# Kernel optimization log

Measured on AMD Instinct MI355X. Metric: run time of the kernel, lower is better.

The kernel has to match this reference:

```python
import jax, jax.numpy as jnp
import numpy as np

FAR = 10.0
RAST = 256          # rast_size default
ORIG_W, ORIG_H = 256.0, 256.0  # orig_size default
CHUNK = 32          # faces processed per scan step
EPS = 1e-9


def _project(vertices, K, R, t, dist):
    # persp projection with lens distortion; vertices [B,V,3] -> [B,V,3] (u,v in [-1,1], z depth)
    v = jnp.einsum('bvj,bij->bvi', vertices, R) + t
    x, y, z = v[..., 0], v[..., 1], v[..., 2]
    x_ = x / (z + EPS)
    y_ = y / (z + EPS)
    k1, k2, p1, p2, k3 = (dist[:, None, i] for i in range(5))
    r2 = x_ * x_ + y_ * y_  # == r**2 in original (r = sqrt(x_^2+y_^2))
    radial = 1.0 + k1 * r2 + k2 * r2 ** 2 + k3 * r2 ** 3
    x__ = x_ * radial + 2.0 * p1 * x_ * y_ + p2 * (r2 + 2.0 * x_ ** 2)
    y__ = y_ * radial + p1 * (r2 + 2.0 * y_ ** 2) + 2.0 * p2 * x_ * y_
    pts = jnp.stack([x__, y__, jnp.ones_like(z)], axis=-1)
    pts = jnp.einsum('bvj,bij->bvi', pts, K)
    u, vv = pts[..., 0], pts[..., 1]
    vv = ORIG_H - vv
    u = 2.0 * (u - ORIG_W / 2.0) / ORIG_W
    vv = 2.0 * (vv - ORIG_H / 2.0) / ORIG_H
    return jnp.stack([u, vv, z], axis=-1)


def _rasterize(fverts):
    # fverts: [B,F,3,3] per-face screen-space vertices (u,v,z). Z-buffer depth raster + coverage mask.
    B, F = fverts.shape[0], fverts.shape[1]
    pad = (-F) % CHUNK
    fv = jnp.pad(fverts, ((0, 0), (0, pad), (0, 0), (0, 0)))  # padded faces are degenerate (den==0)
    nc = (F + pad) // CHUNK
    fv = fv.reshape(B, nc, CHUNK, 3, 3).transpose(1, 0, 2, 3, 4)  # [nc,B,CHUNK,3,3]
    # pixel centers in [-1,1]; row i top-to-bottom maps to y = -1..1 (consistent with flipped v)
    g = 2.0 * (jnp.arange(RAST, dtype=jnp.float32) + 0.5) / RAST - 1.0
    X = g[None, None, None, :]   # cols
    Y = g[None, None, :, None]   # rows

    def body(carry, ch):
        zbuf, cover = carry
        e = lambda i, j: ch[:, :, i, j][:, :, None, None]
        ax, ay, az = e(0, 0), e(0, 1), e(0, 2)
        bx, by, bz = e(1, 0), e(1, 1), e(1, 2)
        cx, cy, cz = e(2, 0), e(2, 1), e(2, 2)
        den = (bx - ax) * (cy - ay) - (by - ay) * (cx - ax)
        ok = jnp.abs(den) > 1e-8
        den_s = jnp.where(ok, den, 1.0)
        # barycentric coords of each pixel wrt this face (signed; fill_back provides both windings)
        w0 = ((by - cy) * (X - cx) + (cx - bx) * (Y - cy)) / den_s
        w1 = ((cy - ay) * (X - cx) + (ax - cx) * (Y - cy)) / den_s
        w2 = 1.0 - w0 - w1
        zs = lambda zz: jnp.where(zz > 1e-8, zz, 1.0)
        inv = w0 / zs(az) + w1 / zs(bz) + w2 / zs(cz)  # perspective-correct 1/z interp
        valid = ok & (w0 >= 0) & (w1 >= 0) & (w2 >= 0)
        valid = valid & (az > 1e-8) & (bz > 1e-8) & (cz > 1e-8) & (inv > 1e-8)
        zp = 1.0 / jnp.where(valid, inv, 1.0)
        zc = jnp.min(jnp.where(valid, zp, FAR), axis=1)  # nearest face in this chunk [B,S,S]
        return (jnp.minimum(zbuf, zc), cover | jnp.any(valid, axis=1)), None

    zbuf0 = jnp.full((B, RAST, RAST), FAR, dtype=jnp.float32)
    cov0 = jnp.zeros((B, RAST, RAST), dtype=bool)
    (zbuf, cover), _ = jax.lax.scan(body, (zbuf0, cov0), fv)
    return zbuf, cover


def _normalize_depth(img, far):
    img_inf = (img == far).astype(jnp.float32)
    img_no_back = (1.0 - img_inf) * img
    img_max = img_no_back.max(axis=1, keepdims=True).max(axis=2, keepdims=True)
    img_min = img.min(axis=1, keepdims=True).min(axis=2, keepdims=True)
    nd = (img_max - img) / (img_max - img_min + 1e-4)
    return jnp.clip(nd, 0.0, 1.0)


def _forward(vertices, faces, intr, R, t, dist_coeffs):
    # fill_back=True: append faces with reversed vertex order
    faces_fb = jnp.concatenate([faces, faces[:, :, ::-1]], axis=1)
    uvz = _project(vertices, intr, R, t, dist_coeffs)
    fverts = jax.vmap(lambda v, f: v[f])(uvz, faces_fb)  # [B,F,3,3]
    zbuf, cover = _rasterize(fverts)
    dep = _normalize_depth(zbuf, FAR)
    mask = cover.astype(jnp.float32)
    return dep, mask


def setup_inputs():
    key = jax.random.key(0)
    k0, k1, k2 = jax.random.split(key, 3)
    B, V, F = 4, 778, 1538  # MANO hand mesh
    vertices = jax.random.normal(k0, (B, V, 3), dtype=jnp.float32) * 0.1 \
        + jnp.array([0.0, 0.0, 0.6], dtype=jnp.float32)  # blob 0.6m in front of camera
    faces = jax.random.randint(k1, (B, F, 3), 0, V, dtype=jnp.int32)
    K = jnp.tile(jnp.array([[500.0, 0.0, 128.0],
                            [0.0, 500.0, 128.0],
                            [0.0, 0.0, 1.0]], dtype=jnp.float32)[None], (B, 1, 1))
    R = jnp.tile(jnp.eye(3, dtype=jnp.float32)[None], (B, 1, 1))
    t = jnp.zeros((B, 1, 3), dtype=jnp.float32)
    dist_coeffs = jax.random.uniform(k2, (B, 5), dtype=jnp.float32) * 0.01
    return {"vertices": vertices, "faces": faces, "intr": K, "R": R, "t": t,
            "dist_coeffs": dist_coeffs}


def reference(vertices, faces, intr, R, t, dist_coeffs):
    return _forward(vertices, faces, intr, R, t, dist_coeffs)
```

## Files before the change

### kernel.cpp

```cpp
#include <hip/hip_runtime.h>
#include <cstdint>

#define RASTN 256
#define FARV 10.0f
#define FARBITS 0x41200000u
#define SPLIT 4
#define NBUCK 1024
#define NINITY 8

__device__ __forceinline__ float gval(int i) {
    return (2.0f * ((float)i + 0.5f)) / 256.0f - 1.0f;
}

__global__ __launch_bounds__(1024) void prep_sort_kernel(
    const float* __restrict__ verts, const int* __restrict__ faces,
    const float* __restrict__ Km, const float* __restrict__ Rm,
    const float* __restrict__ tm, const float* __restrict__ dm,
    float4* __restrict__ rec, uint2* __restrict__ sax, unsigned short* __restrict__ stri,
    unsigned int* __restrict__ zbits, unsigned int* __restrict__ mm,
    float* __restrict__ uvzg, int V, int F, int F2, int B, int npix)
{
#pragma clang fp contract(off)
    __shared__ float s_uvz[1024*3];
    __shared__ unsigned int s_pk[4096];
    __shared__ unsigned short s_bk[4096];
    __shared__ unsigned int s_hist[NBUCK], s_cnt2[NBUCK];
    int b = blockIdx.x, y = blockIdx.y, tid = threadIdx.x;
    uint4* zb4 = (uint4*)(zbits + (size_t)b * npix);
    int n4 = npix >> 2;
    int sl0 = (n4 * y) / NINITY, sl1 = (n4 * (y + 1)) / NINITY;
    for (int i = sl0 + tid; i < sl1; i += 1024)
        zb4[i] = make_uint4(FARBITS, FARBITS, FARBITS, FARBITS);
    if (y > 0) return;
    if (tid == 0) { mm[2*b] = 0u; mm[2*b+1] = FARBITS; }
    for (int i = tid; i < NBUCK; i += 1024) s_hist[i] = 0u;
    bool inlds = (V <= 1024);
    const float* R = Rm + b*9; const float* K = Km + b*9;
    const float* t = tm + b*3; const float* d = dm + b*5;
    for (int v = tid; v < V; v += 1024) {
        float vx = verts[((size_t)b*V + v)*3+0];
        float vy = verts[((size_t)b*V + v)*3+1];
        float vz = verts[((size_t)b*V + v)*3+2];
        float cxm = ((vx*R[0] + vy*R[1]) + vz*R[2]) + t[0];
        float cym = ((vx*R[3] + vy*R[4]) + vz*R[5]) + t[1];
        float czm = ((vx*R[6] + vy*R[7]) + vz*R[8]) + t[2];
        float zd = czm + 1e-9f;
        float x_ = cxm / zd;
        float y_ = cym / zd;
        float k1 = d[0], k2 = d[1], p1 = d[2], p2 = d[3], k3 = d[4];
        float r2   = (x_*x_) + (y_*y_);
        float r2_2 = r2 * r2;
        float r2_3 = r2 * r2_2;
        float radial = ((1.0f + k1*r2) + k2*r2_2) + k3*r2_3;
        float x__ = ((x_*radial) + (((2.0f*p1)*x_)*y_)) + (p2*(r2 + 2.0f*(x_*x_)));
        float y__ = ((y_*radial) + (p1*(r2 + 2.0f*(y_*y_)))) + (((2.0f*p2)*x_)*y_);
        float up = ((x__*K[0]) + (y__*K[1])) + (1.0f*K[2]);
        float vp = ((x__*K[3]) + (y__*K[4])) + (1.0f*K[5]);
        vp = 256.0f - vp;
        float un = (2.0f*(up - 128.0f)) / 256.0f;
        float vn = (2.0f*(vp - 128.0f)) / 256.0f;
        if (inlds) { s_uvz[v*3+0]=un; s_uvz[v*3+1]=vn; s_uvz[v*3+2]=czm; }
        else { uvzg[((size_t)b*V+v)*3+0]=un; uvzg[((size_t)b*V+v)*3+1]=vn; uvzg[((size_t)b*V+v)*3+2]=czm; }
    }
    __syncthreads();
    const float* ub = inlds ? s_uvz : (uvzg + (size_t)b*V*3);
    const int* fb = faces + (size_t)b * F * 3;
    float4* rb = rec + (size_t)b * F2 * 4;
    bool stash = (F2 <= 4096);
    for (int j = tid; j < F2; j += 1024) {
        int i0, i1, i2;
        if (j < F) { i0 = fb[j*3+0]; i1 = fb[j*3+1]; i2 = fb[j*3+2]; }
        else { int jj = j - F; i0 = fb[jj*3+2]; i1 = fb[jj*3+1]; i2 = fb[jj*3+0]; }
        float ax = ub[i0*3+0], ay = ub[i0*3+1], az = ub[i0*3+2];
        float bx = ub[i1*3+0], by = ub[i1*3+1], bz = ub[i1*3+2];
        float cx = ub[i2*3+0], cy = ub[i2*3+1], cz = ub[i2*3+2];
        float den = (bx-ax)*(cy-ay) - (by-ay)*(cx-ax);
        bool ok = fabsf(den) > 1e-8f;
        float dens = ok ? den : 1.0f;
        bool alive = ok && (az > 1e-8f) && (bz > 1e-8f) && (cz > 1e-8f);
        float za = (az > 1e-8f) ? az : 1.0f;
        float zb = (bz > 1e-8f) ? bz : 1.0f;
        float zc = (cz > 1e-8f) ? cz : 1.0f;
        float mnx = fminf(ax, fminf(bx, cx));
        float mxx = fmaxf(ax, fmaxf(bx, cx));
        float mny = fminf(ay, fminf(by, cy));
        float mxy = fmaxf(ay, fmaxf(by, cy));
        float m = 1e-3f + 1e-6f*((fabsf(mnx)+fabsf(mxx))+(fabsf(mny)+fabsf(mxy)));
        mnx -= m; mxx += m; mny -= m; mxy += m;
        if (!(mxx >= -1.0f) || !(mnx <= 1.0f) || !(mxy >= -1.0f) || !(mny <= 1.0f)) alive = false;
        int ic0 = 1, ic1 = 0, ir0 = 1, ir1 = 0;
        float minz = 3e38f;
        if (alive) {
            float lx = fmaxf(mnx, -1.5f), hx = fminf(mxx, 1.5f);
            float ly = fmaxf(mny, -1.5f), hy = fminf(mxy, 1.5f);
            ic0 = (int)floorf((lx + 1.0f) * 128.0f - 0.5f);
            ic1 = (int)ceilf ((hx + 1.0f) * 128.0f - 0.5f);
            ir0 = (int)floorf((ly + 1.0f) * 128.0f - 0.5f);
            ir1 = (int)ceilf ((hy + 1.0f) * 128.0f - 0.5f);
            ic0 = ic0 < 0 ? 0 : ic0;  ir0 = ir0 < 0 ? 0 : ir0;
            ic1 = ic1 > 255 ? 255 : ic1;  ir1 = ir1 > 255 ? 255 : ir1;
            if (ic0 > ic1 || ir0 > ir1) { ic0 = 1; ic1 = 0; ir0 = 1; ir1 = 0; minz = 3e38f; }
            else minz = fminf(za, fminf(zb, zc)) * (1.0f - 4e-4f);
        }
        float minzv = fminf(za, fminf(zb, zc));
        float maxzv = fmaxf(za, fmaxf(zb, zc));
        float rd = __builtin_amdgcn_rcpf(dens);
        float ra, rbz, rc;
        if (minzv > 1e-2f && maxzv < 100.0f * minzv) {
            ra  = __builtin_amdgcn_rcpf(za);
            rbz = __builtin_amdgcn_rcpf(zb);
            rc  = __builtin_amdgcn_rcpf(zc);
        } else {
            ra = rbz = rc = __builtin_huge_valf();
        }
        unsigned int pack = (unsigned int)(ic0 | (ic1 << 8) | (ir0 << 16) | (ir1 << 24));
        int bk = NBUCK - 1;
        if (minz < 1e30f) {
            bk = (int)(minz * 512.0f);
            bk = bk < 0 ? 0 : (bk > NBUCK-2 ? NBUCK-2 : bk);
        }
        size_t base = (size_t)j * 4;
        rb[base+0] = make_float4(cx, cy, by - cy, cx - bx);
        rb[base+1] = make_float4(cy - ay, ax - cx, rd, ra);
        rb[base+2] = make_float4(dens, za, zb, zc);
        rb[base+3] = make_float4(__uint_as_float(pack), minz, rbz, rc);
        atomicAdd(&s_hist[bk], 1u);
        if (stash) { s_pk[j] = pack; s_bk[j] = (unsigned short)bk; }
    }
    __syncthreads();
    for (int i = tid; i < NBUCK; i += 1024) s_cnt2[i] = s_hist[i];
    __syncthreads();
    for (int st = 1; st < NBUCK; st <<= 1) {
        unsigned int v = 0;
        if (tid < NBUCK && tid >= st) v = s_cnt2[tid - st];
        __syncthreads();
        if (tid < NBUCK && tid >= st) s_cnt2[tid] += v;
        __syncthreads();
    }
    if (tid < NBUCK) s_cnt2[tid] -= s_hist[tid];
    __syncthreads();
    uint2* sxb = sax + (size_t)b * F2;
    unsigned short* stb = stri + (size_t)b * F2;
    for (int j = tid; j < F2; j += 1024) {
        unsigned int pack; int bk;
        if (stash) { pack = s_pk[j]; bk = (int)s_bk[j]; }
        else {
            float4 q3 = rb[(size_t)j*4+3];
            pack = __float_as_uint(q3.x);
            float mz = q3.y;
            bk = NBUCK - 1;
            if (mz < 1e30f) { bk = (int)(mz * 512.0f); bk = bk < 0 ? 0 : (bk > NBUCK-2 ? NBUCK-2 : bk); }
        }
        float key = (bk == NBUCK-1) ? 3e38f : (float)bk * (1.0f/512.0f);
        int pos = (int)atomicAdd(&s_cnt2[bk], 1u);
        sxb[pos] = make_uint2(pack, __float_as_uint(key));
        stb[pos] = (unsigned short)j;
    }
}

__global__ __launch_bounds__(256) void raster_kernel(
    const float4* __restrict__ rec, const uint2* __restrict__ sax,
    const unsigned short* __restrict__ stri, unsigned int* __restrict__ zbits,
    int F2)
{
#pragma clang fp contract(off)
    __shared__ float4 sh[256];
    __shared__ float s_mz[64];
    __shared__ int s_bb[64];
    __shared__ unsigned short s_list[256];
    __shared__ int s_wk[4], s_kk[4], s_wo[4];
    __shared__ int s_tot, s_kc;
    __shared__ float s_tzmax, s_red[4];
    int zz = blockIdx.z;
    int b = zz / SPLIT, sp = zz - b*SPLIT;
    int tc = blockIdx.x, tr = blockIdx.y;
    int tid = threadIdx.x, lane = tid & 63, wv = tid >> 6;
    int tx = tid & 15, ty = tid >> 4;
    int col = tc*16 + tx, row = tr*16 + ty;
    float X = gval(col), Y = gval(row);
    int pc0 = tc*16, pc1 = pc0+15, pr0 = tr*16, pr1 = pr0+15;
    const float4* rb = rec + (size_t)b * F2 * 4;
    const uint2* sxb = sax + (size_t)b * F2;
    const unsigned short* stb = stri + (size_t)b * F2;
    size_t pix = ((size_t)b*RASTN + row)*RASTN + col;
    unsigned int* zp_g = zbits + pix;
    float zmin = FARV;
    float pushed = FARV;
    if (tid == 0) s_tzmax = FARV;
    __syncthreads();
    int nch = (F2 + 256*SPLIT - 1) / (256*SPLIT);
    for (int c = 0; c < nch; ++c) {
        int s = (c*256 + tid)*SPLIT + sp;
        bool kp = false, sv = false; unsigned int tri = 0;
        if (s < F2) {
            uint2 a = sxb[s];
            float kf = __uint_as_float(a.y);
            kp = !(kf > s_tzmax);
            if (kp) {
                int pk = (int)a.x;
                int ic0 = pk & 255, ic1 = (pk >> 8) & 255;
                int ir0 = (pk >> 16) & 255, ir1 = (pk >> 24) & 255;
                sv = (ic0 <= ic1) && (ic0 <= pc1) && (ic1 >= pc0) && (ir0 <= pr1) && (ir1 >= pr0);
                if (sv) tri = stb[s];
            }
        }
        unsigned long long bs = __ballot(sv ? 1 : 0);
        unsigned long long bk = __ballot(kp ? 1 : 0);
        int pfx = __popcll(bs & ((1ull << lane) - 1ull));
        if (lane == 0) { s_wk[wv] = __popcll(bs); s_kk[wv] = __popcll(bk); }
        __syncthreads();
        if (tid == 0) {
            int acc = 0;
            for (int q = 0; q < 4; ++q) { s_wo[q] = acc; acc += s_wk[q]; }
            s_tot = acc;
            s_kc = s_kk[0] + s_kk[1] + s_kk[2] + s_kk[3];
        }
        __syncthreads();
        if (sv) s_list[s_wo[wv] + pfx] = (unsigned short)tri;
        int kcnt = s_kc, n = s_tot;
        if (kcnt == 0) break;
        for (int g = 0; g < n; g += 64) {
            __syncthreads();
            int cnt2 = (n - g) < 64 ? (n - g) : 64;
            if (tid < cnt2*4) {
                unsigned int t4 = s_list[g + (tid >> 2)];
                float4 f = rb[(size_t)t4*4 + (tid & 3)];
                sh[tid] = f;
                if ((tid & 3) == 3) {
                    s_mz[tid >> 2] = f.y;
                    s_bb[tid >> 2] = __float_as_int(f.x);
                }
            }
            __syncthreads();
            {
                float zg = __uint_as_float(__hip_atomic_load(
                    zp_g, __ATOMIC_RELAXED, __HIP_MEMORY_SCOPE_AGENT));
                pushed = fminf(pushed, zg);
                zmin = fminf(zmin, zg);
            }
            for (int i = 0; i < cnt2; ++i) {
                float mz = s_mz[i];
                if (mz > zmin) continue;
                int pk = s_bb[i];
                int ic0 = pk & 255, ic1 = (pk >> 8) & 255;
                int ir0 = (pk >> 16) & 255, ir1 = (pk >> 24) & 255;
                if (col < ic0 || col > ic1 || row < ir0 || row > ir1) continue;
                float4 q0 = sh[i*4+0];
                float4 q1 = sh[i*4+1];
                float xc = X - q0.x;
                float yc = Y - q0.y;
                float e0 = (q0.z*xc) + (q0.w*yc);
                float e1 = (q1.x*xc) + (q1.y*yc);
                float rd = q1.z;
                float sgn = copysignf(1.0f, rd);
                float s0 = e0*sgn, s1 = e1*sgn;
                float w0a = e0*rd, w1a = e1*rd;
                float w2a = (1.0f - w0a) - w1a;
                float epsu = 1e-4f*((1.0f + fabsf(w0a)) + fabsf(w1a));
                if (s0 > -1e-30f && s1 > -1e-30f && w2a > -epsu) {
                    float4 q3 = sh[i*4+3];
                    float inva = ((w0a*q1.w) + (w1a*q3.z)) + (w2a*q3.w);
                    float zpa = __builtin_amdgcn_rcpf(inva);
                    bool clearly = (s0 > 0.0f) && (s1 > 0.0f) && (w2a > epsu) && (inva > 1e-6f);
                    if (!clearly || zpa < zmin*1.001f) {
                        float4 q2 = sh[i*4+2];
                        float dens = q2.x;
                        float w0 = e0 / dens;
                        float w1 = e1 / dens;
                        float w2 = (1.0f - w0) - w1;
                        float inv = ((w0 / q2.y) + (w1 / q2.z)) + (w2 / q2.w);
                        if ((w0 >= 0.0f) && (w1 >= 0.0f) && (w2 >= 0.0f) && (inv > 1e-8f)) {
                            float zp = 1.0f / inv;
                            zmin = fminf(zmin, zp);
                        }
                    }
                }
            }
            if (zmin < pushed) {
                atomicMin(zp_g, __float_as_uint(zmin));
                pushed = zmin;
            }
        }
        if (n > 0) {
            float zx = zmin;
            for (int o = 32; o; o >>= 1) zx = fmaxf(zx, __shfl_xor(zx, o));
            if (lane == 0) s_red[wv] = zx;
        }
        __syncthreads();
        if (n > 0 && tid == 0)
            s_tzmax = fminf(s_tzmax,
                fmaxf(fmaxf(s_red[0], s_red[1]), fmaxf(s_red[2], s_red[3])));
        __syncthreads();
    }
    if (zmin < pushed)
        atomicMin(zp_g, __float_as_uint(zmin));
}

__global__ __launch_bounds__(256) void minmax_kernel(
    const float* __restrict__ zbuf, float* __restrict__ mask,
    unsigned int* __restrict__ mm, int npix, int seg)
{
    __shared__ float smx[4], smn[4];
    int b = blockIdx.y;
    size_t base = (size_t)b * npix + (size_t)blockIdx.x * seg;
    const float* p = zbuf + base;
    float* mk = mask + base;
    int lane = threadIdx.x & 63, wv = threadIdx.x >> 6;
    float vmx = 0.0f, vmn = FARV;
    for (int i = threadIdx.x; i < seg; i += 256) {
        float z = p[i];
        mk[i] = (z < FARV) ? 1.0f : 0.0f;
        float nb = (z == FARV) ? 0.0f : z;
        vmx = fmaxf(vmx, nb);
        vmn = fminf(vmn, z);
    }
    for (int o = 32; o; o >>= 1) {
        vmx = fmaxf(vmx, __shfl_xor(vmx, o));
        vmn = fminf(vmn, __shfl_xor(vmn, o));
    }
    if (lane == 0) { smx[wv] = vmx; smn[wv] = vmn; }
    __syncthreads();
    if (threadIdx.x == 0) {
        float bmx = fmaxf(fmaxf(smx[0], smx[1]), fmaxf(smx[2], smx[3]));
        float bmn = fminf(fminf(smn[0], smn[1]), fminf(smn[2], smn[3]));
        atomicMax(mm + 2*b,     __float_as_uint(bmx));
        atomicMin(mm + 2*b + 1, __float_as_uint(bmn));
    }
}

__global__ __launch_bounds__(256) void final_kernel(
    float* __restrict__ zdep, const unsigned int* __restrict__ mm, int npix, int total)
{
#pragma clang fp contract(off)
    int idx = blockIdx.x*256 + threadIdx.x;
    if (idx >= total) return;
    int b = idx / npix;
    float mx = __uint_as_float(mm[2*b]);
    float mn = __uint_as_float(mm[2*b + 1]);
    float z = zdep[idx];
    float nd = (mx - z) / ((mx - mn) + 1e-4f);
    float cv = nd;
    cv = (cv < 0.0f) ? 0.0f : cv;
    cv = (cv > 1.0f) ? 1.0f : cv;
    zdep[idx] = cv;
}

extern "C" void kernel_launch(void* const* d_in, const int* in_sizes, int n_in,
                              void* d_out, int out_size, void* d_ws, size_t ws_size,
                              hipStream_t stream)
{
    const float* verts = (const float*)d_in[0];
    const int*   faces = (const int*)d_in[1];
    const float* Km    = (const float*)d_in[2];
    const float* Rm    = (const float*)d_in[3];
    const float* tm    = (const float*)d_in[4];
    const float* dm    = (const float*)d_in[5];
    float* out = (float*)d_out;

    int B  = in_sizes[2] / 9;
    int V  = in_sizes[0] / (3 * B);
    int F  = in_sizes[1] / (3 * B);
    int F2 = 2 * F;
    int npix = RASTN * RASTN;

    char* ws = (char*)d_ws;
    size_t off = 0;
    float4* rec = (float4*)(ws + off);
    off = (off + (size_t)B * F2 * 4 * sizeof(float4) + 255) & ~(size_t)255;
    uint2* sax = (uint2*)(ws + off);
    off = (off + (size_t)B * F2 * sizeof(uint2) + 255) & ~(size_t)255;
    unsigned short* stri = (unsigned short*)(ws + off);
    off = (off + (size_t)B * F2 * sizeof(unsigned short) + 255) & ~(size_t)255;
    float* uvzg = (float*)(ws + off);
    off = (off + (size_t)B * V * 3 * sizeof(float) + 255) & ~(size_t)255;
    unsigned int* mm = (unsigned int*)(ws + off);

    unsigned int* zbits = (unsigned int*)out;
    float* mask = out + (size_t)B * npix;

    dim3 pgrid(B, NINITY);
    prep_sort_kernel<<<pgrid, 1024, 0, stream>>>(
        verts, faces, Km, Rm, tm, dm, rec, sax, stri, zbits, mm, uvzg,
        V, F, F2, B, npix);
    dim3 rgrid(16, 16, B * SPLIT);
    raster_kernel<<<rgrid, 256, 0, stream>>>(rec, sax, stri, zbits, F2);
    int seg = npix / 16;
    dim3 mgrid(16, B);
    minmax_kernel<<<mgrid, 256, 0, stream>>>((float*)zbits, mask, mm, npix, seg);
    final_kernel<<<(B * npix + 255) / 256, 256, 0, stream>>>((float*)zbits, mm, npix, B * npix);
}
```

Measured before the change: 178.3 us.

## Double-buffer raster face staging, wave-shuffle scan, vectorize minmax and final passes

After: 182.1 us. 1.02x slower.

```diff
diff --git a/kernel.cpp b/kernel.cpp
--- a/kernel.cpp
+++ b/kernel.cpp
@@ -25,7 +25,9 @@
     __shared__ unsigned int s_pk[4096];
     __shared__ unsigned short s_bk[4096];
     __shared__ unsigned int s_hist[NBUCK], s_cnt2[NBUCK];
+    __shared__ unsigned int s_ws[16];
     int b = blockIdx.x, y = blockIdx.y, tid = threadIdx.x;
+    int lane = tid & 63, wv16 = tid >> 6;
     uint4* zb4 = (uint4*)(zbits + (size_t)b * npix);
     int n4 = npix >> 2;
     int sl0 = (n4 * y) / NINITY, sl1 = (n4 * (y + 1)) / NINITY;
@@ -128,16 +130,27 @@
         if (stash) { s_pk[j] = pack; s_bk[j] = (unsigned short)bk; }
     }
     __syncthreads();
-    for (int i = tid; i < NBUCK; i += 1024) s_cnt2[i] = s_hist[i];
-    __syncthreads();
-    for (int st = 1; st < NBUCK; st <<= 1) {
-        unsigned int v = 0;
-        if (tid < NBUCK && tid >= st) v = s_cnt2[tid - st];
-        __syncthreads();
-        if (tid < NBUCK && tid >= st) s_cnt2[tid] += v;
-        __syncthreads();
-    }
-    if (tid < NBUCK) s_cnt2[tid] -= s_hist[tid];
+    {
+        unsigned int h = s_hist[tid];
+        unsigned int v = h;
+        for (int o = 1; o < 64; o <<= 1) {
+            unsigned int tsh = __shfl_up(v, o, 64);
+            if (lane >= o) v += tsh;
+        }
+        if (lane == 63) s_ws[wv16] = v;
+        __syncthreads();
+        if (tid < 16) {
+            unsigned int w = s_ws[tid];
+            for (int o = 1; o < 16; o <<= 1) {
+                unsigned int tsh = __shfl_up(w, o, 64);
+                if (tid >= o) w += tsh;
+            }
+            s_ws[tid] = w;
+        }
+        __syncthreads();
+        unsigned int add = (wv16 > 0) ? s_ws[wv16 - 1] : 0u;
+        s_cnt2[tid] = v + add - h;
+    }
     __syncthreads();
     uint2* sxb = sax + (size_t)b * F2;
     unsigned short* stb = stri + (size_t)b * F2;
@@ -164,9 +177,8 @@
     int F2)
 {
 #pragma clang fp contract(off)
-    __shared__ float4 sh[256];
-    __shared__ float s_mz[64];
-    __shared__ int s_bb[64];
+    __shared__ float4 sh[2][256];
+    __shared__ float2 s_mzbb[2][64];
     __shared__ unsigned short s_list[256];
     __shared__ int s_wk[4], s_kk[4], s_wo[4];
     __shared__ int s_tot, s_kc;
@@ -219,34 +231,50 @@
         if (sv) s_list[s_wo[wv] + pfx] = (unsigned short)tri;
         int kcnt = s_kc, n = s_tot;
         if (kcnt == 0) break;
-        for (int g = 0; g < n; g += 64) {
-            __syncthreads();
+        float zg = __uint_as_float(__hip_atomic_load(
+            zp_g, __ATOMIC_RELAXED, __HIP_MEMORY_SCOPE_AGENT));
+        __syncthreads();
+        int ngrp = (n + 63) >> 6;
+        if (n > 0) {
+            int cnt0 = n < 64 ? n : 64;
+            if (tid < cnt0*4) {
+                unsigned int t4 = s_list[tid >> 2];
+                float4 f = rb[(size_t)t4*4 + (tid & 3)];
+                sh[0][tid] = f;
+                if ((tid & 3) == 3) s_mzbb[0][tid >> 2] = make_float2(f.y, f.x);
+            }
+        }
+        __syncthreads();
+        for (int gi = 0; gi < ngrp; ++gi) {
+            int buf = gi & 1;
+            pushed = fminf(pushed, zg);
+            zmin = fminf(zmin, zg);
+            float zg_n = __uint_as_float(__hip_atomic_load(
+                zp_g, __ATOMIC_RELAXED, __HIP_MEMORY_SCOPE_AGENT));
+            float4 fpref = make_float4(0.f, 0.f, 0.f, 0.f);
+            bool hp = false;
+            if (gi + 1 < ngrp) {
+                int g2 = (gi + 1) << 6;
+                int cnt3 = (n - g2) < 64 ? (n - g2) : 64;
+                if (tid < cnt3*4) {
+                    unsigned int t4 = s_list[g2 + (tid >> 2)];
+                    fpref = rb[(size_t)t4*4 + (tid & 3)];
+                    hp = true;
+                }
+            }
+            int g = gi << 6;
             int cnt2 = (n - g) < 64 ? (n - g) : 64;
-            if (tid < cnt2*4) {
-                unsigned int t4 = s_list[g + (tid >> 2)];
-                float4 f = rb[(size_t)t4*4 + (tid & 3)];
-                sh[tid] = f;
-                if ((tid & 3) == 3) {
-                    s_mz[tid >> 2] = f.y;
-                    s_bb[tid >> 2] = __float_as_int(f.x);
-                }
-            }
-            __syncthreads();
-            {
-                float zg = __uint_as_float(__hip_atomic_load(
-                    zp_g, __ATOMIC_RELAXED, __HIP_MEMORY_SCOPE_AGENT));
-                pushed = fminf(pushed, zg);
-                zmin = fminf(zmin, zg);
-            }
+            float2 nx = s_mzbb[buf][0];
             for (int i = 0; i < cnt2; ++i) {
-                float mz = s_mz[i];
+                float mz = nx.x;
+                int pk = __float_as_int(nx.y);
+                nx = s_mzbb[buf][(i + 1) & 63];
                 if (mz > zmin) continue;
-                int pk = s_bb[i];
                 int ic0 = pk & 255, ic1 = (pk >> 8) & 255;
                 int ir0 = (pk >> 16) & 255, ir1 = (pk >> 24) & 255;
                 if (col < ic0 || col > ic1 || row < ir0 || row > ir1) continue;
-                float4 q0 = sh[i*4+0];
-                float4 q1 = sh[i*4+1];
+                float4 q0 = sh[buf][i*4+0];
+                float4 q1 = sh[buf][i*4+1];
                 float xc = X - q0.x;
                 float yc = Y - q0.y;
                 float e0 = (q0.z*xc) + (q0.w*yc);
@@ -258,12 +286,12 @@
                 float w2a = (1.0f - w0a) - w1a;
                 float epsu = 1e-4f*((1.0f + fabsf(w0a)) + fabsf(w1a));
                 if (s0 > -1e-30f && s1 > -1e-30f && w2a > -epsu) {
-                    float4 q3 = sh[i*4+3];
+                    float4 q3 = sh[buf][i*4+3];
                     float inva = ((w0a*q1.w) + (w1a*q3.z)) + (w2a*q3.w);
                     float zpa = __builtin_amdgcn_rcpf(inva);
                     bool clearly = (s0 > 0.0f) && (s1 > 0.0f) && (w2a > epsu) && (inva > 1e-6f);
                     if (!clearly || zpa < zmin*1.001f) {
-                        float4 q2 = sh[i*4+2];
+                        float4 q2 = sh[buf][i*4+2];
                         float dens = q2.x;
                         float w0 = e0 / dens;
                         float w1 = e1 / dens;
@@ -280,6 +308,12 @@
                 atomicMin(zp_g, __float_as_uint(zmin));
                 pushed = zmin;
             }
+            zg = zg_n;
+            if (hp) {
+                sh[buf ^ 1][tid] = fpref;
+                if ((tid & 3) == 3) s_mzbb[buf ^ 1][tid >> 2] = make_float2(fpref.y, fpref.x);
+            }
+            __syncthreads();
         }
         if (n > 0) {
             float zx = zmin;
@@ -297,23 +331,26 @@
 }
 
 __global__ __launch_bounds__(256) void minmax_kernel(
-    const float* __restrict__ zbuf, float* __restrict__ mask,
-    unsigned int* __restrict__ mm, int npix, int seg)
+    const float4* __restrict__ zbuf, float4* __restrict__ mask,
+    unsigned int* __restrict__ mm, int npix)
 {
     __shared__ float smx[4], smn[4];
     int b = blockIdx.y;
-    size_t base = (size_t)b * npix + (size_t)blockIdx.x * seg;
-    const float* p = zbuf + base;
-    float* mk = mask + base;
+    size_t i4 = (((size_t)b * npix) >> 2) + (size_t)blockIdx.x * 256 + threadIdx.x;
+    float4 z = zbuf[i4];
+    float4 mk;
+    mk.x = (z.x < FARV) ? 1.0f : 0.0f;
+    mk.y = (z.y < FARV) ? 1.0f : 0.0f;
+    mk.z = (z.z < FARV) ? 1.0f : 0.0f;
+    mk.w = (z.w < FARV) ? 1.0f : 0.0f;
+    mask[i4] = mk;
+    float nbx = (z.x == FARV) ? 0.0f : z.x;
+    float nby = (z.y == FARV) ? 0.0f : z.y;
+    float nbz = (z.z == FARV) ? 0.0f : z.z;
+    float nbw = (z.w == FARV) ? 0.0f : z.w;
+    float vmx = fmaxf(fmaxf(nbx, nby), fmaxf(nbz, nbw));
+    float vmn = fminf(fminf(z.x, z.y), fminf(z.z, z.w));
     int lane = threadIdx.x & 63, wv = threadIdx.x >> 6;
-    float vmx = 0.0f, vmn = FARV;
-    for (int i = threadIdx.x; i < seg; i += 256) {
-        float z = p[i];
-        mk[i] = (z < FARV) ? 1.0f : 0.0f;
-        float nb = (z == FARV) ? 0.0f : z;
-        vmx = fmaxf(vmx, nb);
-        vmn = fminf(vmn, z);
-    }
     for (int o = 32; o; o >>= 1) {
         vmx = fmaxf(vmx, __shfl_xor(vmx, o));
         vmn = fminf(vmn, __shfl_xor(vmn, o));
@@ -329,20 +366,27 @@
 }
 
 __global__ __launch_bounds__(256) void final_kernel(
-    float* __restrict__ zdep, const unsigned int* __restrict__ mm, int npix, int total)
+    float4* __restrict__ zdep, const unsigned int* __restrict__ mm,
+    int npix4, int total4)
 {
 #pragma clang fp contract(off)
     int idx = blockIdx.x*256 + threadIdx.x;
-    if (idx >= total) return;
-    int b = idx / npix;
+    if (idx >= total4) return;
+    int b = idx / npix4;
     float mx = __uint_as_float(mm[2*b]);
     float mn = __uint_as_float(mm[2*b + 1]);
-    float z = zdep[idx];
-    float nd = (mx - z) / ((mx - mn) + 1e-4f);
-    float cv = nd;
-    cv = (cv < 0.0f) ? 0.0f : cv;
-    cv = (cv > 1.0f) ? 1.0f : cv;
-    zdep[idx] = cv;
+    float den = (mx - mn) + 1e-4f;
+    float4 z = zdep[idx];
+    float4 r;
+    r.x = (mx - z.x) / den;
+    r.y = (mx - z.y) / den;
+    r.z = (mx - z.z) / den;
+    r.w = (mx - z.w) / den;
+    r.x = r.x < 0.0f ? 0.0f : (r.x > 1.0f ? 1.0f : r.x);
+    r.y = r.y < 0.0f ? 0.0f : (r.y > 1.0f ? 1.0f : r.y);
+    r.z = r.z < 0.0f ? 0.0f : (r.z > 1.0f ? 1.0f : r.z);
+    r.w = r.w < 0.0f ? 0.0f : (r.w > 1.0f ? 1.0f : r.w);
+    zdep[idx] = r;
 }
 
 extern "C" void kernel_launch(void* const* d_in, const int* in_sizes, int n_in,
@@ -384,8 +428,11 @@
         V, F, F2, B, npix);
     dim3 rgrid(16, 16, B * SPLIT);
     raster_kernel<<<rgrid, 256, 0, stream>>>(rec, sax, stri, zbits, F2);
-    int seg = npix / 16;
-    dim3 mgrid(16, B);
-    minmax_kernel<<<mgrid, 256, 0, stream>>>((float*)zbits, mask, mm, npix, seg);
-    final_kernel<<<(B * npix + 255) / 256, 256, 0, stream>>>((float*)zbits, mm, npix, B * npix);
-}
+    dim3 mgrid(npix / 1024, B);
+    minmax_kernel<<<mgrid, 256, 0, stream>>>(
+        (const float4*)zbits, (float4*)mask, mm, npix);
+    int npix4 = npix >> 2;
+    int total4 = B * npix4;
+    final_kernel<<<(total4 + 255) / 256, 256, 0, stream>>>(
+        (float4*)zbits, mm, npix4, total4);
+}
```
